# Performance work log

Measured on AMD Instinct MI355X. Metric: run time of the kernel, lower is better.

## Reference

```python
import jax, jax.numpy as jnp
import numpy as np

N, C, D, H, W = 1, 32, 64, 192, 160


def affine_grid_3d(theta, size):
    # PyTorch F.affine_grid 3D, align_corners=True convention.
    n, c, d, h, w = size
    z = jnp.linspace(-1.0, 1.0, d)
    y = jnp.linspace(-1.0, 1.0, h)
    x = jnp.linspace(-1.0, 1.0, w)
    zz, yy, xx = jnp.meshgrid(z, y, x, indexing='ij')          # [D,H,W]
    base = jnp.stack([xx, yy, zz, jnp.ones_like(xx)], axis=-1)  # [D,H,W,4]
    return jnp.einsum('dhwk,nck->ndhwc', base, theta)           # [N,D,H,W,3] (x,y,z)


def _gather_corner(vol, zi, yi, xi):
    # vol: [C,D,H,W]; zi/yi/xi: [D,H,W] int32. Zero padding outside.
    c, d, h, w = vol.shape
    valid = (zi >= 0) & (zi < d) & (yi >= 0) & (yi < h) & (xi >= 0) & (xi < w)
    zc = jnp.clip(zi, 0, d - 1)
    yc = jnp.clip(yi, 0, h - 1)
    xc = jnp.clip(xi, 0, w - 1)
    flat = vol.reshape(c, d * h * w)
    idx = (zc * h + yc) * w + xc
    vals = jnp.take(flat, idx.reshape(-1), axis=1).reshape(c, *zi.shape)
    return vals * valid[None].astype(vol.dtype)


def grid_sample_3d(inp, grid):
    # Trilinear grid_sample, zeros padding, align_corners=True.
    n, c, d, h, w = inp.shape
    x = (grid[..., 0] + 1.0) * 0.5 * (w - 1)
    y = (grid[..., 1] + 1.0) * 0.5 * (h - 1)
    z = (grid[..., 2] + 1.0) * 0.5 * (d - 1)
    x0 = jnp.floor(x).astype(jnp.int32); x1 = x0 + 1
    y0 = jnp.floor(y).astype(jnp.int32); y1 = y0 + 1
    z0 = jnp.floor(z).astype(jnp.int32); z1 = z0 + 1
    wx = (x - x0.astype(x.dtype))
    wy = (y - y0.astype(y.dtype))
    wz = (z - z0.astype(z.dtype))

    def sample_one(vol, z0, z1, y0, y1, x0, x1, wz, wy, wx):
        out = jnp.zeros((vol.shape[0],) + wz.shape, dtype=vol.dtype)
        for zi, wzc in ((z0, 1.0 - wz), (z1, wz)):
            for yi, wyc in ((y0, 1.0 - wy), (y1, wy)):
                for xi, wxc in ((x0, 1.0 - wx), (x1, wx)):
                    out = out + _gather_corner(vol, zi, yi, xi) * (wzc * wyc * wxc)[None]
        return out

    return jax.vmap(sample_one)(inp, z0, z1, y0, y1, x0, x1, wz, wy, wx)


def setup_inputs() -> dict:
    key = jax.random.key(0)
    k1, k2 = jax.random.split(key)
    inp = jax.random.normal(k1, (N, C, D, H, W), dtype=jnp.float32)
    identity = jnp.asarray([1, 0, 0, 0, 0, 1, 0, 0, 0, 0, 1, 0], dtype=jnp.float32)
    theta = identity + 0.1 * jax.random.normal(k2, (12,), dtype=jnp.float32)
    return {"input": inp, "theta": theta}


def reference(input, theta):
    th = theta.reshape(1, 3, 4)
    grid = affine_grid_3d(th, input.shape)       # [N,D,H,W,3]
    out = grid_sample_3d(input, grid)            # [N,C,D,H,W]
    return jnp.transpose(out, (0, 4, 3, 1, 2))   # [N,W,H,C,D]
```

## Files before the change

### kernel.cpp

```cpp
#include <hip/hip_runtime.h>

constexpr int W_ = 160;
constexpr int H_ = 192;
constexpr int D_ = 64;
constexpr int C_ = 32;
constexpr int HW_  = H_ * W_;
constexpr int DHWi = D_ * HW_;
constexpr int CD   = C_ * D_;

constexpr int TW = 16, TH = 8, TD = 16;
constexpr int NWT = W_ / TW;
constexpr int NHT = H_ / TH;
constexpr int NDT = D_ / TD;
constexpr int QPP = NWT * NHT;
constexpr int CPX = C_ / 8;
constexpr int BXF   = 32;
constexpr int RMAX  = 420;
constexpr int LROWS = RMAX + 2;

typedef float f4_t __attribute__((ext_vector_type(4)));
typedef float f2_t __attribute__((ext_vector_type(2)));

__global__ void __launch_bounds__(256, 4)
affine_grid_sample_kernel(const float* __restrict__ inp,
                          const float* __restrict__ th,
                          float* __restrict__ out)
{
    __shared__ float Lb[BXF * LROWS];

    const int t   = threadIdx.x;
    const int bid = blockIdx.x;
    const int xcd = bid & 7;
    const int r_  = bid >> 3;
    const int q   = r_ % QPP;
    const int rem = r_ / QPP;
    const int c   = xcd * CPX + (rem >> 2);
    const int dt  = rem & 3;
    const int hs  = q / NWT;
    const int wt  = q - hs * NWT;
    const int w0 = wt * TW, h0 = hs * TH, d0 = dt * TD;

    const float th0=th[0], th1=th[1], th2 =th[2],  th3 =th[3];
    const float th4=th[4], th5=th[5], th6 =th[6],  th7 =th[7];
    const float th8=th[8], th9=th[9], th10=th[10], th11=th[11];

    const float* __restrict__ pc = inp + (size_t)c * DHWi;

    float pxmn= 1e30f, pxmx=-1e30f, pymn= 1e30f, pymx=-1e30f,
          pzmn= 1e30f, pzmx=-1e30f;
    #pragma unroll
    for (int ci = 0; ci < 8; ++ci) {
        const int cw = (ci & 1) ? w0 + TW - 1 : w0;
        const int chh= (ci & 2) ? h0 + TH - 1 : h0;
        const int cd = (ci & 4) ? d0 + TD - 1 : d0;
        const float zzc = fmaf((float)cd, 2.0f / (D_ - 1), -1.0f);
        const float kxc = fmaf(th2,  zzc, th3);
        const float kyc = fmaf(th6,  zzc, th7);
        const float kzc = fmaf(th10, zzc, th11);
        const float xxc = fmaf((float)cw,  2.0f / (W_ - 1), -1.0f);
        const float yyc = fmaf((float)chh, 2.0f / (H_ - 1), -1.0f);
        const float px = (fmaf(th0, xxc, fmaf(th1, yyc, kxc)) + 1.0f) * (0.5f * (W_ - 1));
        const float py = (fmaf(th4, xxc, fmaf(th5, yyc, kyc)) + 1.0f) * (0.5f * (H_ - 1));
        const float pz = (fmaf(th8, xxc, fmaf(th9, yyc, kzc)) + 1.0f) * (0.5f * (D_ - 1));
        pxmn = fminf(pxmn, px); pxmx = fmaxf(pxmx, px);
        pymn = fminf(pymn, py); pymx = fmaxf(pymx, py);
        pzmn = fminf(pzmn, pz); pzmx = fmaxf(pzmx, pz);
    }
    const int xlo = max((int)floorf(pxmn), 0);
    const int xhi = min((int)floorf(pxmx) + 1, W_ - 1);
    const int ylo = max((int)floorf(pymn), 0);
    const int yhi = min((int)floorf(pymx) + 1, H_ - 1);
    const int zlo = max((int)floorf(pzmn), 0);
    const int zhi = min((int)floorf(pzmx) + 1, D_ - 1);
    const int BXr = xhi - xlo + 1;
    const int BYr = yhi - ylo + 1;
    const int BZr = zhi - zlo + 1;
    const int R   = BZr * BYr;
    const bool fits = (BXr <= BXF) && (BYr <= 128) && (R <= RMAX);

    if (fits) {
        const int lane = t & 63, wv = t >> 6;
        const int half = lane >> 5;
        const int lx   = lane & 31;
        const unsigned m18 = (262144u + (unsigned)BYr - 1) / (unsigned)BYr;
        const int npair = (R + 1) >> 1;
        for (int p = wv; p < npair; p += 4) {
            const int rr = 2 * p + half;
            const int bz = (int)(((unsigned)rr * m18) >> 18);
            const int by = rr - bz * BYr;
            const int gz = min(zlo + bz, D_ - 1);
            const int gy = min(ylo + by, H_ - 1);
            const int gx = min(xlo + lx, W_ - 1);
            const float* gsrc = pc + ((unsigned)(gz * HW_ + gy * W_ + gx));
            __builtin_amdgcn_global_load_lds(
                (const __attribute__((address_space(1))) unsigned*)gsrc,
                (__attribute__((address_space(3))) unsigned*)&Lb[(2 * p) * BXF],
                4, 0, 0);
        }
        asm volatile("s_waitcnt vmcnt(0)" ::: "memory");
    }
    __syncthreads();

    const int dq = t & 1;
    const int wl = (t >> 1) & 15;
    const int hl = t >> 5;
    const int w  = w0 + wl;
    const int h  = h0 + hl;
    const float xx = fmaf((float)w, 2.0f / (W_ - 1), -1.0f);
    const float yy = fmaf((float)h, 2.0f / (H_ - 1), -1.0f);

    f4_t val0, val1;
    #pragma unroll
    for (int k = 0; k < 8; ++k) {
        const int d = d0 + (k & 3) + dq * 4 + (k >> 2) * 8;
        const float zz  = fmaf((float)d, 2.0f / (D_ - 1), -1.0f);
        const float kzx = fmaf(th2,  zz, th3);
        const float kzy = fmaf(th6,  zz, th7);
        const float kzz = fmaf(th10, zz, th11);
        const float px = (fmaf(th0, xx, fmaf(th1, yy, kzx)) + 1.0f) * (0.5f * (W_ - 1));
        const float py = (fmaf(th4, xx, fmaf(th5, yy, kzy)) + 1.0f) * (0.5f * (H_ - 1));
        const float pz = (fmaf(th8, xx, fmaf(th9, yy, kzz)) + 1.0f) * (0.5f * (D_ - 1));
        const float fx = floorf(px), fy = floorf(py), fz = floorf(pz);
        const int ix0 = (int)fx, iy0 = (int)fy, iz0 = (int)fz;
        const float wx = px - fx, wy = py - fy, wz = pz - fz;
        const float u0r = ((unsigned)ix0       < (unsigned)W_) ? (1.0f - wx) : 0.0f;
        const float u1r = ((unsigned)(ix0 + 1) < (unsigned)W_) ? wx          : 0.0f;
        const float v0  = ((unsigned)iy0       < (unsigned)H_) ? (1.0f - wy) : 0.0f;
        const float v1  = ((unsigned)(iy0 + 1) < (unsigned)H_) ? wy          : 0.0f;
        const float s0  = ((unsigned)iz0       < (unsigned)D_) ? (1.0f - wz) : 0.0f;
        const float s1  = ((unsigned)(iz0 + 1) < (unsigned)D_) ? wz          : 0.0f;
        float wA = u0r, wB = u1r;
        if (ix0 == -1)     { wA = u1r; wB = 0.0f; }
        if (ix0 == W_ - 1) { wA = 0.0f; wB = u0r; }
        const int e   = min(max(ix0,     0), W_ - 2);
        const int cy0 = min(max(iy0,     0), H_ - 1);
        const int cy1 = min(max(iy0 + 1, 0), H_ - 1);
        const int cz0 = min(max(iz0,     0), D_ - 1);
        const int cz1 = min(max(iz0 + 1, 0), D_ - 1);

        float a00, b00, a01, b01, a10, b10, a11, b11;
        if (__builtin_expect(fits, 1)) {
            const int bx  = e - xlo;
            const int r00 = (cz0 - zlo) * BYr + (cy0 - ylo);
            const int r01 = (cz0 - zlo) * BYr + (cy1 - ylo);
            const int r10 = (cz1 - zlo) * BYr + (cy0 - ylo);
            const int r11 = (cz1 - zlo) * BYr + (cy1 - ylo);
            const float* L00 = &Lb[(r00 << 5) + bx];
            const float* L01 = &Lb[(r01 << 5) + bx];
            const float* L10 = &Lb[(r10 << 5) + bx];
            const float* L11 = &Lb[(r11 << 5) + bx];
            a00 = L00[0]; b00 = L00[1];
            a01 = L01[0]; b01 = L01[1];
            a10 = L10[0]; b10 = L10[1];
            a11 = L11[0]; b11 = L11[1];
        } else {
            f2_t P0, P1, P2, P3;
            const unsigned o0 = (unsigned)(cz0 * HW_ + cy0 * W_ + e);
            const unsigned o1 = (unsigned)(cz0 * HW_ + cy1 * W_ + e);
            const unsigned o2 = (unsigned)(cz1 * HW_ + cy0 * W_ + e);
            const unsigned o3 = (unsigned)(cz1 * HW_ + cy1 * W_ + e);
            __builtin_memcpy(&P0, pc + o0, 8);
            __builtin_memcpy(&P1, pc + o1, 8);
            __builtin_memcpy(&P2, pc + o2, 8);
            __builtin_memcpy(&P3, pc + o3, 8);
            asm volatile("" :: "v"(P0), "v"(P1), "v"(P2), "v"(P3));
            a00 = P0[0]; b00 = P0[1]; a01 = P1[0]; b01 = P1[1];
            a10 = P2[0]; b10 = P2[1]; a11 = P3[0]; b11 = P3[1];
        }

        const float x00 = wA * a00 + wB * b00;
        const float x01 = wA * a01 + wB * b01;
        const float x10 = wA * a10 + wB * b10;
        const float x11 = wA * a11 + wB * b11;
        const float e0 = v0 * x00 + v1 * x01;
        const float e1 = v0 * x10 + v1 * x11;
        const float v  = s0 * e0 + s1 * e1;
        if (k < 4) val0[k] = v; else val1[k - 4] = v;
    }

    float* const ob = out + ((size_t)w * H_ + h) * CD + (size_t)c * D_ + d0 + dq * 4;
    __builtin_nontemporal_store(val0, (f4_t*)ob);
    __builtin_nontemporal_store(val1, (f4_t*)(ob + 8));
}

extern "C" void kernel_launch(void* const* d_in, const int* in_sizes, int n_in,
                              void* d_out, int out_size, void* d_ws, size_t ws_size,
                              hipStream_t stream)
{
    const float* inp = (const float*)d_in[0];
    const float* th  = (const float*)d_in[1];
    float* out = (float*)d_out;

    hipLaunchKernelGGL(affine_grid_sample_kernel, dim3(8 * CPX * NDT * QPP),
                       dim3(256), 0, stream, inp, th, out);
}
```

Before: 640.1 us.

## Pad LDS row stride to 33 and add interior fast path without bounds checks

Changes the shared-memory tile layout from a 32-float row stride to a padded 33-float stride, aiming to reduce bank conflicts on the trilinear gathers. The staging loop now uses 33 lanes per row with incremental z/y indexing instead of a magic-number division. A specialised path for tiles whose footprint lies fully inside the volume drops all clamping and validity masking. Each thread now writes 8 contiguous depths (two adjacent float4 stores) instead of two strided groups, which changes the output write pattern. The cost is code duplication across three branches and slightly higher register and LDS pressure.

```diff
diff --git a/kernel.cpp b/kernel.cpp
--- a/kernel.cpp
+++ b/kernel.cpp
@@ -14,9 +14,8 @@
 constexpr int NDT = D_ / TD;
 constexpr int QPP = NWT * NHT;
 constexpr int CPX = C_ / 8;
-constexpr int BXF   = 32;
-constexpr int RMAX  = 420;
-constexpr int LROWS = RMAX + 2;
+constexpr int LSTR = 33;
+constexpr int RMAX = 408;
 
 typedef float f4_t __attribute__((ext_vector_type(4)));
 typedef float f2_t __attribute__((ext_vector_type(2)));
@@ -26,7 +25,7 @@
                           const float* __restrict__ th,
                           float* __restrict__ out)
 {
-    __shared__ float Lb[BXF * LROWS];
+    __shared__ float Lb[RMAX * LSTR];
 
     const int t   = threadIdx.x;
     const int bid = blockIdx.x;
@@ -43,6 +42,7 @@
     const float th0=th[0], th1=th[1], th2 =th[2],  th3 =th[3];
     const float th4=th[4], th5=th[5], th6 =th[6],  th7 =th[7];
     const float th8=th[8], th9=th[9], th10=th[10], th11=th[11];
+    const float CX = 0.5f * (W_ - 1), CY = 0.5f * (H_ - 1), CZ = 0.5f * (D_ - 1);
 
     const float* __restrict__ pc = inp + (size_t)c * DHWi;
 
@@ -59,43 +59,43 @@
         const float kzc = fmaf(th10, zzc, th11);
         const float xxc = fmaf((float)cw,  2.0f / (W_ - 1), -1.0f);
         const float yyc = fmaf((float)chh, 2.0f / (H_ - 1), -1.0f);
-        const float px = (fmaf(th0, xxc, fmaf(th1, yyc, kxc)) + 1.0f) * (0.5f * (W_ - 1));
-        const float py = (fmaf(th4, xxc, fmaf(th5, yyc, kyc)) + 1.0f) * (0.5f * (H_ - 1));
-        const float pz = (fmaf(th8, xxc, fmaf(th9, yyc, kzc)) + 1.0f) * (0.5f * (D_ - 1));
+        const float px = fmaf(fmaf(th0, xxc, fmaf(th1, yyc, kxc)), CX, CX);
+        const float py = fmaf(fmaf(th4, xxc, fmaf(th5, yyc, kyc)), CY, CY);
+        const float pz = fmaf(fmaf(th8, xxc, fmaf(th9, yyc, kzc)), CZ, CZ);
         pxmn = fminf(pxmn, px); pxmx = fmaxf(pxmx, px);
         pymn = fminf(pymn, py); pymx = fmaxf(pymx, py);
         pzmn = fminf(pzmn, pz); pzmx = fmaxf(pzmx, pz);
     }
-    const int xlo = max((int)floorf(pxmn), 0);
-    const int xhi = min((int)floorf(pxmx) + 1, W_ - 1);
-    const int ylo = max((int)floorf(pymn), 0);
-    const int yhi = min((int)floorf(pymx) + 1, H_ - 1);
-    const int zlo = max((int)floorf(pzmn), 0);
-    const int zhi = min((int)floorf(pzmx) + 1, D_ - 1);
+    const int xlo_u = (int)floorf(pxmn), xhi_u = (int)floorf(pxmx) + 1;
+    const int ylo_u = (int)floorf(pymn), yhi_u = (int)floorf(pymx) + 1;
+    const int zlo_u = (int)floorf(pzmn), zhi_u = (int)floorf(pzmx) + 1;
+    const int xlo = max(xlo_u, 0), xhi = min(xhi_u, W_ - 1);
+    const int ylo = max(ylo_u, 0), yhi = min(yhi_u, H_ - 1);
+    const int zlo = max(zlo_u, 0), zhi = min(zhi_u, D_ - 1);
     const int BXr = xhi - xlo + 1;
     const int BYr = yhi - ylo + 1;
     const int BZr = zhi - zlo + 1;
     const int R   = BZr * BYr;
-    const bool fits = (BXr <= BXF) && (BYr <= 128) && (R <= RMAX);
+    const bool fits = (BXr <= 32) && (BYr >= 4) && (R <= RMAX);
+    const bool interior = (xlo_u >= 0) && (xhi_u <= W_ - 1) &&
+                          (ylo_u >= 0) && (yhi_u <= H_ - 1) &&
+                          (zlo_u >= 0) && (zhi_u <= D_ - 1);
 
     if (fits) {
-        const int lane = t & 63, wv = t >> 6;
-        const int half = lane >> 5;
-        const int lx   = lane & 31;
-        const unsigned m18 = (262144u + (unsigned)BYr - 1) / (unsigned)BYr;
-        const int npair = (R + 1) >> 1;
-        for (int p = wv; p < npair; p += 4) {
-            const int rr = 2 * p + half;
-            const int bz = (int)(((unsigned)rr * m18) >> 18);
-            const int by = rr - bz * BYr;
-            const int gz = min(zlo + bz, D_ - 1);
-            const int gy = min(ylo + by, H_ - 1);
-            const int gx = min(xlo + lx, W_ - 1);
-            const float* gsrc = pc + ((unsigned)(gz * HW_ + gy * W_ + gx));
-            __builtin_amdgcn_global_load_lds(
-                (const __attribute__((address_space(1))) unsigned*)gsrc,
-                (__attribute__((address_space(3))) unsigned*)&Lb[(2 * p) * BXF],
-                4, 0, 0);
+        const int lane = t & 63;
+        const int wv   = t >> 6;
+        if (lane < 33) {
+            const float* __restrict__ pl = pc + min(xlo + lane, W_ - 1);
+            int bz = 0, by = wv;
+            for (int rr = wv; rr < R; rr += 4) {
+                const int go = (zlo + bz) * HW_ + (ylo + by) * W_;
+                __builtin_amdgcn_global_load_lds(
+                    (const __attribute__((address_space(1))) unsigned*)(pl + go),
+                    (__attribute__((address_space(3))) unsigned*)&Lb[rr * LSTR],
+                    4, 0, 0);
+                by += 4;
+                if (by >= BYr) { by -= BYr; ++bz; }
+            }
         }
         asm volatile("s_waitcnt vmcnt(0)" ::: "memory");
     }
@@ -108,79 +108,134 @@
     const int h  = h0 + hl;
     const float xx = fmaf((float)w, 2.0f / (W_ - 1), -1.0f);
     const float yy = fmaf((float)h, 2.0f / (H_ - 1), -1.0f);
+    const int db = d0 + dq * 8;
 
     f4_t val0, val1;
-    #pragma unroll
-    for (int k = 0; k < 8; ++k) {
-        const int d = d0 + (k & 3) + dq * 4 + (k >> 2) * 8;
-        const float zz  = fmaf((float)d, 2.0f / (D_ - 1), -1.0f);
-        const float kzx = fmaf(th2,  zz, th3);
-        const float kzy = fmaf(th6,  zz, th7);
-        const float kzz = fmaf(th10, zz, th11);
-        const float px = (fmaf(th0, xx, fmaf(th1, yy, kzx)) + 1.0f) * (0.5f * (W_ - 1));
-        const float py = (fmaf(th4, xx, fmaf(th5, yy, kzy)) + 1.0f) * (0.5f * (H_ - 1));
-        const float pz = (fmaf(th8, xx, fmaf(th9, yy, kzz)) + 1.0f) * (0.5f * (D_ - 1));
-        const float fx = floorf(px), fy = floorf(py), fz = floorf(pz);
-        const int ix0 = (int)fx, iy0 = (int)fy, iz0 = (int)fz;
-        const float wx = px - fx, wy = py - fy, wz = pz - fz;
-        const float u0r = ((unsigned)ix0       < (unsigned)W_) ? (1.0f - wx) : 0.0f;
-        const float u1r = ((unsigned)(ix0 + 1) < (unsigned)W_) ? wx          : 0.0f;
-        const float v0  = ((unsigned)iy0       < (unsigned)H_) ? (1.0f - wy) : 0.0f;
-        const float v1  = ((unsigned)(iy0 + 1) < (unsigned)H_) ? wy          : 0.0f;
-        const float s0  = ((unsigned)iz0       < (unsigned)D_) ? (1.0f - wz) : 0.0f;
-        const float s1  = ((unsigned)(iz0 + 1) < (unsigned)D_) ? wz          : 0.0f;
-        float wA = u0r, wB = u1r;
-        if (ix0 == -1)     { wA = u1r; wB = 0.0f; }
-        if (ix0 == W_ - 1) { wA = 0.0f; wB = u0r; }
-        const int e   = min(max(ix0,     0), W_ - 2);
-        const int cy0 = min(max(iy0,     0), H_ - 1);
-        const int cy1 = min(max(iy0 + 1, 0), H_ - 1);
-        const int cz0 = min(max(iz0,     0), D_ - 1);
-        const int cz1 = min(max(iz0 + 1, 0), D_ - 1);
-
-        float a00, b00, a01, b01, a10, b10, a11, b11;
-        if (__builtin_expect(fits, 1)) {
+    const int PS = BYr * LSTR;
+
+    if (fits && interior) {
+        #pragma unroll
+        for (int k = 0; k < 8; ++k) {
+            const int d = db + k;
+            const float zz  = fmaf((float)d, 2.0f / (D_ - 1), -1.0f);
+            const float kzx = fmaf(th2,  zz, th3);
+            const float kzy = fmaf(th6,  zz, th7);
+            const float kzz = fmaf(th10, zz, th11);
+            const float px = fmaf(fmaf(th0, xx, fmaf(th1, yy, kzx)), CX, CX);
+            const float py = fmaf(fmaf(th4, xx, fmaf(th5, yy, kzy)), CY, CY);
+            const float pz = fmaf(fmaf(th8, xx, fmaf(th9, yy, kzz)), CZ, CZ);
+            const float fx = floorf(px), fy = floorf(py), fz = floorf(pz);
+            const int ix0 = (int)fx, iy0 = (int)fy, iz0 = (int)fz;
+            const float wx = px - fx, wy = py - fy, wz = pz - fz;
+            const float u0 = 1.0f - wx, v0 = 1.0f - wy, s0 = 1.0f - wz;
+            const int bx = ix0 - xlo;
+            const int ry = iy0 - ylo;
+            const int rz = iz0 - zlo;
+            const int a0 = rz * PS + ry * LSTR + bx;
+            const int a1 = a0 + PS;
+            const float a00 = Lb[a0],        b00 = Lb[a0 + 1];
+            const float a01 = Lb[a0 + LSTR], b01 = Lb[a0 + LSTR + 1];
+            const float a10 = Lb[a1],        b10 = Lb[a1 + 1];
+            const float a11 = Lb[a1 + LSTR], b11 = Lb[a1 + LSTR + 1];
+            const float x00 = u0 * a00 + wx * b00;
+            const float x01 = u0 * a01 + wx * b01;
+            const float x10 = u0 * a10 + wx * b10;
+            const float x11 = u0 * a11 + wx * b11;
+            const float e0 = v0 * x00 + wy * x01;
+            const float e1 = v0 * x10 + wy * x11;
+            const float v  = s0 * e0 + wz * e1;
+            if (k < 4) val0[k] = v; else val1[k - 4] = v;
+        }
+    } else if (fits) {
+        #pragma unroll
+        for (int k = 0; k < 8; ++k) {
+            const int d = db + k;
+            const float zz  = fmaf((float)d, 2.0f / (D_ - 1), -1.0f);
+            const float kzx = fmaf(th2,  zz, th3);
+            const float kzy = fmaf(th6,  zz, th7);
+            const float kzz = fmaf(th10, zz, th11);
+            const float px = fmaf(fmaf(th0, xx, fmaf(th1, yy, kzx)), CX, CX);
+            const float py = fmaf(fmaf(th4, xx, fmaf(th5, yy, kzy)), CY, CY);
+            const float pz = fmaf(fmaf(th8, xx, fmaf(th9, yy, kzz)), CZ, CZ);
+            const float fx = floorf(px), fy = floorf(py), fz = floorf(pz);
+            const int ix0 = (int)fx, iy0 = (int)fy, iz0 = (int)fz;
+            const float wx = px - fx, wy = py - fy, wz = pz - fz;
+            const float u0r = ((unsigned)ix0       < (unsigned)W_) ? (1.0f - wx) : 0.0f;
+            const float u1r = ((unsigned)(ix0 + 1) < (unsigned)W_) ? wx          : 0.0f;
+            const float v0  = ((unsigned)iy0       < (unsigned)H_) ? (1.0f - wy) : 0.0f;
+            const float v1  = ((unsigned)(iy0 + 1) < (unsigned)H_) ? wy          : 0.0f;
+            const float s0  = ((unsigned)iz0       < (unsigned)D_) ? (1.0f - wz) : 0.0f;
+            const float s1  = ((unsigned)(iz0 + 1) < (unsigned)D_) ? wz          : 0.0f;
+            float wA = u0r, wB = u1r;
+            if (ix0 == -1)     { wA = u1r; wB = 0.0f; }
+            if (ix0 == W_ - 1) { wA = 0.0f; wB = u0r; }
+            const int e   = min(max(ix0,     0), W_ - 2);
+            const int cy0 = min(max(iy0,     0), H_ - 1);
+            const int cy1 = min(max(iy0 + 1, 0), H_ - 1);
+            const int cz0 = min(max(iz0,     0), D_ - 1);
+            const int cz1 = min(max(iz0 + 1, 0), D_ - 1);
             const int bx  = e - xlo;
-            const int r00 = (cz0 - zlo) * BYr + (cy0 - ylo);
-            const int r01 = (cz0 - zlo) * BYr + (cy1 - ylo);
-            const int r10 = (cz1 - zlo) * BYr + (cy0 - ylo);
-            const int r11 = (cz1 - zlo) * BYr + (cy1 - ylo);
-            const float* L00 = &Lb[(r00 << 5) + bx];
-            const float* L01 = &Lb[(r01 << 5) + bx];
-            const float* L10 = &Lb[(r10 << 5) + bx];
-            const float* L11 = &Lb[(r11 << 5) + bx];
-            a00 = L00[0]; b00 = L00[1];
-            a01 = L01[0]; b01 = L01[1];
-            a10 = L10[0]; b10 = L10[1];
-            a11 = L11[0]; b11 = L11[1];
-        } else {
+            const int a00i = (cz0 - zlo) * PS + (cy0 - ylo) * LSTR + bx;
+            const int a01i = (cz0 - zlo) * PS + (cy1 - ylo) * LSTR + bx;
+            const int a10i = (cz1 - zlo) * PS + (cy0 - ylo) * LSTR + bx;
+            const int a11i = (cz1 - zlo) * PS + (cy1 - ylo) * LSTR + bx;
+            const float x00 = wA * Lb[a00i] + wB * Lb[a00i + 1];
+            const float x01 = wA * Lb[a01i] + wB * Lb[a01i + 1];
+            const float x10 = wA * Lb[a10i] + wB * Lb[a10i + 1];
+            const float x11 = wA * Lb[a11i] + wB * Lb[a11i + 1];
+            const float e0 = v0 * x00 + v1 * x01;
+            const float e1 = v0 * x10 + v1 * x11;
+            const float v  = s0 * e0 + s1 * e1;
+            if (k < 4) val0[k] = v; else val1[k - 4] = v;
+        }
+    } else {
+        #pragma unroll
+        for (int k = 0; k < 8; ++k) {
+            const int d = db + k;
+            const float zz  = fmaf((float)d, 2.0f / (D_ - 1), -1.0f);
+            const float kzx = fmaf(th2,  zz, th3);
+            const float kzy = fmaf(th6,  zz, th7);
+            const float kzz = fmaf(th10, zz, th11);
+            const float px = fmaf(fmaf(th0, xx, fmaf(th1, yy, kzx)), CX, CX);
+            const float py = fmaf(fmaf(th4, xx, fmaf(th5, yy, kzy)), CY, CY);
+            const float pz = fmaf(fmaf(th8, xx, fmaf(th9, yy, kzz)), CZ, CZ);
+            const float fx = floorf(px), fy = floorf(py), fz = floorf(pz);
+            const int ix0 = (int)fx, iy0 = (int)fy, iz0 = (int)fz;
+            const float wx = px - fx, wy = py - fy, wz = pz - fz;
+            const float u0r = ((unsigned)ix0       < (unsigned)W_) ? (1.0f - wx) : 0.0f;
+            const float u1r = ((unsigned)(ix0 + 1) < (unsigned)W_) ? wx          : 0.0f;
+            const float v0  = ((unsigned)iy0       < (unsigned)H_) ? (1.0f - wy) : 0.0f;
+            const float v1  = ((unsigned)(iy0 + 1) < (unsigned)H_) ? wy          : 0.0f;
+            const float s0  = ((unsigned)iz0       < (unsigned)D_) ? (1.0f - wz) : 0.0f;
+            const float s1  = ((unsigned)(iz0 + 1) < (unsigned)D_) ? wz          : 0.0f;
+            float wA = u0r, wB = u1r;
+            if (ix0 == -1)     { wA = u1r; wB = 0.0f; }
+            if (ix0 == W_ - 1) { wA = 0.0f; wB = u0r; }
+            const int e   = min(max(ix0,     0), W_ - 2);
+            const int cy0 = min(max(iy0,     0), H_ - 1);
+            const int cy1 = min(max(iy0 + 1, 0), H_ - 1);
+            const int cz0 = min(max(iz0,     0), D_ - 1);
+            const int cz1 = min(max(iz0 + 1, 0), D_ - 1);
             f2_t P0, P1, P2, P3;
-            const unsigned o0 = (unsigned)(cz0 * HW_ + cy0 * W_ + e);
-            const unsigned o1 = (unsigned)(cz0 * HW_ + cy1 * W_ + e);
-            const unsigned o2 = (unsigned)(cz1 * HW_ + cy0 * W_ + e);
-            const unsigned o3 = (unsigned)(cz1 * HW_ + cy1 * W_ + e);
-            __builtin_memcpy(&P0, pc + o0, 8);
-            __builtin_memcpy(&P1, pc + o1, 8);
-            __builtin_memcpy(&P2, pc + o2, 8);
-            __builtin_memcpy(&P3, pc + o3, 8);
+            __builtin_memcpy(&P0, pc + (unsigned)(cz0 * HW_ + cy0 * W_ + e), 8);
+            __builtin_memcpy(&P1, pc + (unsigned)(cz0 * HW_ + cy1 * W_ + e), 8);
+            __builtin_memcpy(&P2, pc + (unsigned)(cz1 * HW_ + cy0 * W_ + e), 8);
+            __builtin_memcpy(&P3, pc + (unsigned)(cz1 * HW_ + cy1 * W_ + e), 8);
             asm volatile("" :: "v"(P0), "v"(P1), "v"(P2), "v"(P3));
-            a00 = P0[0]; b00 = P0[1]; a01 = P1[0]; b01 = P1[1];
-            a10 = P2[0]; b10 = P2[1]; a11 = P3[0]; b11 = P3[1];
-        }
-
-        const float x00 = wA * a00 + wB * b00;
-        const float x01 = wA * a01 + wB * b01;
-        const float x10 = wA * a10 + wB * b10;
-        const float x11 = wA * a11 + wB * b11;
-        const float e0 = v0 * x00 + v1 * x01;
-        const float e1 = v0 * x10 + v1 * x11;
-        const float v  = s0 * e0 + s1 * e1;
-        if (k < 4) val0[k] = v; else val1[k - 4] = v;
+            const float x00 = wA * P0[0] + wB * P0[1];
+            const float x01 = wA * P1[0] + wB * P1[1];
+            const float x10 = wA * P2[0] + wB * P2[1];
+            const float x11 = wA * P3[0] + wB * P3[1];
+            const float e0 = v0 * x00 + v1 * x01;
+            const float e1 = v0 * x10 + v1 * x11;
+            const float v  = s0 * e0 + s1 * e1;
+            if (k < 4) val0[k] = v; else val1[k - 4] = v;
+        }
     }
 
-    float* const ob = out + ((size_t)w * H_ + h) * CD + (size_t)c * D_ + d0 + dq * 4;
+    float* const ob = out + ((size_t)w * H_ + h) * CD + (size_t)c * D_ + db;
     __builtin_nontemporal_store(val0, (f4_t*)ob);
-    __builtin_nontemporal_store(val1, (f4_t*)(ob + 8));
+    __builtin_nontemporal_store(val1, (f4_t*)(ob + 4));
 }
 
 extern "C" void kernel_launch(void* const* d_in, const int* in_sizes, int n_in,
```

After: 711.6 us. 1.11x slower.
